# Performance work log

Hardware: AMD Instinct MI355X
Metric: run time of the kernel (lower is better)

## Reference

```python
import jax, jax.numpy as jnp
import numpy as np
from jax import lax

N_NODES = 100000
N_EDGES = 600000  # even: edges stored as consecutive reverse pairs
NODE_F = 64
EDGE_F = 16
EDGE_H = 128
NODE_H = 128
NUM_STEPS = 6


def setup_inputs() -> dict:
    key = jax.random.key(0)
    ks = jax.random.split(key, 16)
    # paired reverse edges: edge 2k is (src,dst), edge 2k+1 is (dst,src)
    src = jax.random.randint(ks[0], (N_EDGES // 2,), 0, N_NODES, dtype=jnp.int32)
    dst = jax.random.randint(ks[1], (N_EDGES // 2,), 0, N_NODES, dtype=jnp.int32)
    from_nodes = jnp.stack([src, dst], axis=1).reshape(-1)
    to_nodes = jnp.stack([dst, src], axis=1).reshape(-1)
    edges = jnp.stack([from_nodes, to_nodes], axis=0)
    return {
        "node_features": jax.random.normal(ks[2], (N_NODES, NODE_F), jnp.float32),
        "edge_features": jax.random.normal(ks[3], (N_EDGES, EDGE_F), jnp.float32),
        "edge_hiddens": jnp.zeros((N_EDGES, EDGE_H), jnp.float32),
        "edges": edges,
        "W1_w": jax.random.normal(ks[4], (NODE_F, EDGE_H), jnp.float32) / np.sqrt(NODE_F),
        "W1_b": jnp.zeros((EDGE_H,), jnp.float32),
        "W2_w": jax.random.normal(ks[5], (EDGE_F, EDGE_H), jnp.float32) / np.sqrt(EDGE_F),
        "W2_b": jnp.zeros((EDGE_H,), jnp.float32),
        "W3_w": jax.random.normal(ks[6], (EDGE_H, EDGE_H), jnp.float32) / np.sqrt(EDGE_H),
        "W3_b": jnp.zeros((EDGE_H,), jnp.float32),
        "U1_w": jax.random.normal(ks[7], (NODE_F, NODE_H), jnp.float32) / np.sqrt(NODE_F),
        "U1_b": jnp.zeros((NODE_H,), jnp.float32),
        "U2_w": jax.random.normal(ks[8], (EDGE_H, NODE_H), jnp.float32) / np.sqrt(EDGE_H),
        "U2_b": jnp.zeros((NODE_H,), jnp.float32),
    }


def reference(node_features, edge_features, edge_hiddens, edges,
              W1_w, W1_b, W2_w, W2_b, W3_w, W3_b, U1_w, U1_b, U2_w, U2_b):
    from_nodes = edges[0]
    to_nodes = edges[1]
    n_edges = edges.shape[1]
    # backlink of edge i is its reverse pair: even i -> i+1, odd i -> i-1
    idx = jnp.arange(n_edges)
    backlink = idx + ((idx + 1) % 2) * 2 - 1

    # loop-invariant terms
    W1_x_u = (node_features @ W1_w + W1_b)[from_nodes]     # [E, EH]
    W2_x_uv = edge_features @ W2_w + W2_b                  # [E, EH]

    def step(h, _):
        # sum edge hiddens by source node, gather back per-edge, drop backlink
        s = jax.ops.segment_sum(h, from_nodes, num_segments=N_NODES)  # [N, EH]
        wu = s[from_nodes] - h[backlink]                               # [E, EH]
        h_new = jax.nn.relu(W1_x_u + W2_x_uv + (wu @ W3_w + W3_b))
        return h_new, None

    edge_h, _ = lax.scan(step, edge_hiddens, None, length=NUM_STEPS)

    U1_x_u = node_features @ U1_w + U1_b                   # [N, NH]
    U2_vu = edge_h @ U2_w + U2_b                           # [E, NH]
    agg = jax.ops.segment_sum(U2_vu, to_nodes, num_segments=N_NODES)
    node_hiddens = jax.nn.relu(U1_x_u + agg)               # [N, NH]
    return node_hiddens
```

## Files before the change

### kernel.cpp

```cpp
#include <hip/hip_runtime.h>
#include <hip/hip_bf16.h>

#define N_NODES 100000
#define N_EDGES 600000
#define SCAN_BLOCKS ((N_NODES + 255) / 256)

typedef __bf16 bf16;
typedef __bf16 bf16x2 __attribute__((ext_vector_type(2)));
typedef __bf16 bf16x4 __attribute__((ext_vector_type(4)));
typedef __bf16 bf16x8 __attribute__((ext_vector_type(8)));
typedef float f32x4 __attribute__((ext_vector_type(4)));

__global__ void deg_hist(const int* __restrict__ from, int* __restrict__ deg, int E) {
    int e = blockIdx.x * blockDim.x + threadIdx.x;
    if (e < E) atomicAdd(&deg[from[e]], 1);
}

__global__ __launch_bounds__(256) void block_sums(
    const int* __restrict__ deg, int* __restrict__ bsum)
{
    __shared__ int s[256];
    int i = blockIdx.x * 256 + threadIdx.x;
    s[threadIdx.x] = (i < N_NODES) ? deg[i] : 0;
    __syncthreads();
    for (int st = 128; st > 0; st >>= 1) {
        if (threadIdx.x < st) s[threadIdx.x] += s[threadIdx.x + st];
        __syncthreads();
    }
    if (threadIdx.x == 0) bsum[blockIdx.x] = s[0];
}

__global__ __launch_bounds__(256) void scan_partials(
    const int* __restrict__ bsum, int* __restrict__ bpref, int* __restrict__ off)
{
    __shared__ int s[SCAN_BLOCKS];
    for (int i = threadIdx.x; i < SCAN_BLOCKS; i += 256) s[i] = bsum[i];
    __syncthreads();
    if (threadIdx.x == 0) {
        int run = 0;
        for (int i = 0; i < SCAN_BLOCKS; i++) { int t = s[i]; s[i] = run; run += t; }
        off[N_NODES] = run;
    }
    __syncthreads();
    for (int i = threadIdx.x; i < SCAN_BLOCKS; i += 256) bpref[i] = s[i];
}

__global__ __launch_bounds__(256) void block_scan(
    const int* __restrict__ deg, const int* __restrict__ bpref,
    int* __restrict__ off, int* __restrict__ cursor)
{
    __shared__ int s[256];
    int i = blockIdx.x * 256 + threadIdx.x;
    int v = (i < N_NODES) ? deg[i] : 0;
    s[threadIdx.x] = v;
    __syncthreads();
    for (int st = 1; st < 256; st <<= 1) {
        int x = (threadIdx.x >= st) ? s[threadIdx.x - st] : 0;
        __syncthreads();
        s[threadIdx.x] += x;
        __syncthreads();
    }
    if (i < N_NODES) {
        int o = bpref[blockIdx.x] + s[threadIdx.x] - v;
        off[i] = o;
        cursor[i] = o;
    }
}

__global__ void scatter_csr(const int* __restrict__ from, int* __restrict__ cursor,
                            int* __restrict__ se, int* __restrict__ rank, int E) {
    int e = blockIdx.x * blockDim.x + threadIdx.x;
    if (e < E) {
        int p = atomicAdd(&cursor[from[e]], 1);
        se[p] = e;
        rank[e] = p;
    }
}

__global__ void make_maps(const int* __restrict__ se, const int* __restrict__ from,
                          const int* __restrict__ rank,
                          int* __restrict__ fromP, int* __restrict__ backP, int E) {
    int i = blockIdx.x * blockDim.x + threadIdx.x;
    if (i < E) {
        int e = se[i];
        fromP[i] = from[e];
        backP[i] = rank[e ^ 1];
    }
}

__global__ __launch_bounds__(256) void node_gemm(
    const float* __restrict__ A, const float* __restrict__ B,
    const float* __restrict__ bias, float* __restrict__ C, int M)
{
    __shared__ float As[16][65];
    __shared__ float Bs[16][128];
    int row0 = blockIdx.x * 64;
    int tid = threadIdx.x;
    int tx = tid & 15, ty = tid >> 4;
    float acc[4][8];
    #pragma unroll
    for (int i = 0; i < 4; i++)
        #pragma unroll
        for (int j = 0; j < 8; j++) acc[i][j] = 0.f;

    for (int kk = 0; kk < 64; kk += 16) {
        int m  = tid >> 2;
        int k4 = (tid & 3) * 4;
        float4 v = make_float4(0.f, 0.f, 0.f, 0.f);
        if (row0 + m < M)
            v = *(const float4*)(A + (size_t)(row0 + m) * 64 + kk + k4);
        As[k4 + 0][m] = v.x; As[k4 + 1][m] = v.y;
        As[k4 + 2][m] = v.z; As[k4 + 3][m] = v.w;
        #pragma unroll
        for (int t = 0; t < 2; t++) {
            int id = tid + t * 256;
            int k = id >> 5, n4 = (id & 31) * 4;
            *(float4*)(&Bs[k][n4]) = *(const float4*)(B + (size_t)(kk + k) * 128 + n4);
        }
        __syncthreads();
        #pragma unroll
        for (int k = 0; k < 16; k++) {
            float a[4], b[8];
            #pragma unroll
            for (int i = 0; i < 4; i++) a[i] = As[k][ty * 4 + i];
            #pragma unroll
            for (int j = 0; j < 8; j++) b[j] = Bs[k][tx + j * 16];
            #pragma unroll
            for (int i = 0; i < 4; i++)
                #pragma unroll
                for (int j = 0; j < 8; j++) acc[i][j] += a[i] * b[j];
        }
        __syncthreads();
    }
    #pragma unroll
    for (int i = 0; i < 4; i++) {
        int r = row0 + ty * 4 + i;
        if (r < M) {
            #pragma unroll
            for (int j = 0; j < 8; j++) {
                int c = tx + j * 16;
                C[(size_t)r * 128 + c] = acc[i][j] + bias[c];
            }
        }
    }
}

__global__ __launch_bounds__(256) void base_sorted(
    const float* __restrict__ nodeW1, const int* __restrict__ fromP,
    const int* __restrict__ se, const float* __restrict__ ef,
    const float* __restrict__ W2, const float* __restrict__ W2b,
    const float* __restrict__ W3b, bf16* __restrict__ baseP)
{
    int tid = threadIdx.x;
    int c0 = (tid & 31) * 4;
    int sub = tid >> 5;
    float4 w[16];
    #pragma unroll
    for (int k = 0; k < 16; k++) w[k] = *(const float4*)(W2 + k * 128 + c0);
    float4 bias;
    {
        float4 a = *(const float4*)(W2b + c0);
        float4 b = *(const float4*)(W3b + c0);
        bias = make_float4(a.x + b.x, a.y + b.y, a.z + b.z, a.w + b.w);
    }
    #pragma unroll 1
    for (int it = 0; it < 64; ++it) {
        int i = blockIdx.x * 512 + it * 8 + sub;
        if (i >= N_EDGES) break;
        const float* efr = ef + (size_t)se[i] * 16;
        float4 nv = *(const float4*)(nodeW1 + (size_t)fromP[i] * 128 + c0);
        float4 acc = make_float4(bias.x + nv.x, bias.y + nv.y,
                                 bias.z + nv.z, bias.w + nv.w);
        #pragma unroll
        for (int k = 0; k < 16; k++) {
            float s = efr[k];
            acc.x += s * w[k].x; acc.y += s * w[k].y;
            acc.z += s * w[k].z; acc.w += s * w[k].w;
        }
        bf16x4 o;
        o[0] = (bf16)acc.x; o[1] = (bf16)acc.y; o[2] = (bf16)acc.z; o[3] = (bf16)acc.w;
        *(bf16x4*)(baseP + (size_t)i * 128 + c0) = o;
    }
}

__global__ __launch_bounds__(256) void prep_weights(
    const float* __restrict__ W3, const float* __restrict__ U2,
    bf16* __restrict__ W3T, bf16* __restrict__ U2T)
{
    int i = blockIdx.x * 256 + threadIdx.x;
    if (i < 128 * 128) {
        int k = i >> 7, n = i & 127;
        W3T[n * 128 + k] = (bf16)W3[k * 128 + n];
        U2T[n * 128 + k] = (bf16)U2[k * 128 + n];
    }
}

__global__ __launch_bounds__(256) void edge_mfma_v2(
    const bf16* __restrict__ baseP, const bf16* __restrict__ gin,
    const bf16* __restrict__ S, const int* __restrict__ fromP,
    const int* __restrict__ backP, const bf16* __restrict__ BT,
    bf16* __restrict__ gout, int fused)
{
    __shared__ bf16 Bsw[128 * 128];
    int tid = threadIdx.x;

    #pragma unroll
    for (int t = 0; t < 8; t++) {
        int c = tid + t * 256;
        int cmr = c & 15;
        int cq  = (c >> 4) & 3;
        int ckt = (c >> 6) & 3;
        int cn  = c >> 8;
        int brow = cn * 16 + cmr;
        int bcol = ckt * 32 + cq * 8;
        *(bf16x8*)&Bsw[(size_t)c * 8] =
            *(const bf16x8*)(BT + (size_t)brow * 128 + bcol);
    }
    __syncthreads();

    int wave = tid >> 6, lane = tid & 63;
    int quad = lane >> 4, mr = lane & 15;

    #pragma unroll 1
    for (int it = 0; it < 4; ++it) {
        int i0 = blockIdx.x * 256 + wave * 64 + it * 16;
        if (i0 >= N_EDGES) break;
        int i = i0 + mr;

        bf16x8 afr[4];
        if (!fused) {
            #pragma unroll
            for (int kt = 0; kt < 4; kt++) {
                bf16x8 bb = *(const bf16x8*)(baseP + (size_t)i * 128 + kt * 32 + quad * 8);
                #pragma unroll
                for (int j = 0; j < 8; j++)
                    afr[kt][j] = (bf16)fmaxf((float)bb[j], 0.f);
            }
        } else {
            const bf16* sr = S   + (size_t)fromP[i] * 128;
            const bf16* gr = gin + (size_t)backP[i] * 128;
            #pragma unroll
            for (int kt = 0; kt < 4; kt++) {
                int c = kt * 32 + quad * 8;
                bf16x8 bb = *(const bf16x8*)(baseP + (size_t)i * 128 + c);
                bf16x8 gg = *(const bf16x8*)(gr + c);
                bf16x8 ss = *(const bf16x8*)(sr + c);
                #pragma unroll
                for (int j = 0; j < 8; j++) {
                    float v = (float)bb[j] + (float)ss[j] - (float)gg[j];
                    afr[kt][j] = (bf16)fmaxf(v, 0.f);
                }
            }
        }

        f32x4 acc[8];
        #pragma unroll
        for (int n = 0; n < 8; n++) acc[n] = (f32x4){0.f, 0.f, 0.f, 0.f};
        #pragma unroll
        for (int kt = 0; kt < 4; kt++) {
            #pragma unroll
            for (int n = 0; n < 8; n++) {
                bf16x8 b = *(const bf16x8*)&Bsw[(size_t)(((n * 4 + kt) * 64) + lane) * 8];
                acc[n] = __builtin_amdgcn_mfma_f32_16x16x32_bf16(afr[kt], b, acc[n], 0, 0, 0);
            }
        }

        #pragma unroll
        for (int np = 0; np < 4; np++) {
            int n0 = np * 2;
            #pragma unroll
            for (int reg = 0; reg < 4; reg++) {
                float v0 = acc[n0][reg], v1 = acc[n0 + 1][reg];
                float o0 = __shfl_xor(v0, 1);
                float o1 = __shfl_xor(v1, 1);
                bf16x2 pk;
                int colb;
                if ((mr & 1) == 0) {
                    pk[0] = (bf16)v0; pk[1] = (bf16)o0;
                    colb = n0 * 16 + mr;
                } else {
                    pk[0] = (bf16)o1; pk[1] = (bf16)v1;
                    colb = (n0 + 1) * 16 + (mr ^ 1);
                }
                int row = i0 + quad * 4 + reg;
                *(bf16x2*)(gout + (size_t)row * 128 + colb) = pk;
            }
        }
    }
}

__global__ __launch_bounds__(256) void segsum_stream(
    const bf16* __restrict__ g, const int* __restrict__ off, bf16* __restrict__ S)
{
    int n = blockIdx.x * 4 + (threadIdx.x >> 6);
    if (n >= N_NODES) return;
    int lane = threadIdx.x & 63;
    int o0 = off[n], o1 = off[n + 1];
    float a0 = 0.f, a1 = 0.f;
    for (int i = o0; i < o1; ++i) {
        bf16x2 v = *(const bf16x2*)(g + (size_t)i * 128 + lane * 2);
        a0 += (float)v[0];
        a1 += (float)v[1];
    }
    bf16x2 o; o[0] = (bf16)a0; o[1] = (bf16)a1;
    *(bf16x2*)(S + (size_t)n * 128 + lane * 2) = o;
}

__global__ __launch_bounds__(256) void segsum_final(
    const bf16* __restrict__ g, const int* __restrict__ off,
    const int* __restrict__ backP, float* __restrict__ agg)
{
    int n = blockIdx.x * 4 + (threadIdx.x >> 6);
    if (n >= N_NODES) return;
    int lane = threadIdx.x & 63;
    int o0 = off[n], o1 = off[n + 1];
    float a0 = 0.f, a1 = 0.f;
    for (int i = o0; i < o1; ++i) {
        int e = backP[i];
        bf16x2 v = *(const bf16x2*)(g + (size_t)e * 128 + lane * 2);
        a0 += (float)v[0];
        a1 += (float)v[1];
    }
    *(float2*)(agg + (size_t)n * 128 + lane * 2) = make_float2(a0, a1);
}

__global__ __launch_bounds__(256) void final_out(
    const float* __restrict__ U1x, const float* __restrict__ agg,
    const int* __restrict__ deg, const float* __restrict__ U2b,
    float* __restrict__ out)
{
    int gid = blockIdx.x * 256 + threadIdx.x;
    int n  = gid >> 5;
    if (n >= N_NODES) return;
    int c4 = gid & 31;
    float d = (float)deg[n];
    float4 a  = *(const float4*)(U1x + (size_t)n * 128 + c4 * 4);
    float4 ag = *(const float4*)(agg + (size_t)n * 128 + c4 * 4);
    float4 ub = *(const float4*)(U2b + c4 * 4);
    float4 r;
    r.x = fmaxf(a.x + ag.x + d * ub.x, 0.f);
    r.y = fmaxf(a.y + ag.y + d * ub.y, 0.f);
    r.z = fmaxf(a.z + ag.z + d * ub.z, 0.f);
    r.w = fmaxf(a.w + ag.w + d * ub.w, 0.f);
    *(float4*)(out + (size_t)n * 128 + c4 * 4) = r;
}

extern "C" void kernel_launch(void* const* d_in, const int* in_sizes, int n_in,
                              void* d_out, int out_size, void* d_ws, size_t ws_size,
                              hipStream_t stream) {
    const float* nf  = (const float*)d_in[0];
    const float* ef  = (const float*)d_in[1];
    const int* edges = (const int*)d_in[3];
    const int* from  = edges;
    const float* W1w = (const float*)d_in[4];
    const float* W1b = (const float*)d_in[5];
    const float* W2w = (const float*)d_in[6];
    const float* W2b = (const float*)d_in[7];
    const float* W3w = (const float*)d_in[8];
    const float* W3b = (const float*)d_in[9];
    const float* U1w = (const float*)d_in[10];
    const float* U1b = (const float*)d_in[11];
    const float* U2w = (const float*)d_in[12];
    const float* U2b = (const float*)d_in[13];
    float* out = (float*)d_out;

    const size_t NODE_MAT = (size_t)N_NODES * 128;
    const size_t EDGE_MAT = (size_t)N_EDGES * 128;
    char* w = (char*)d_ws;
    float* nodeW1 = (float*)w; w += NODE_MAT * 4;
    float* agg    = (float*)w; w += NODE_MAT * 4;
    bf16*  S      = (bf16*)w;  w += NODE_MAT * 2;
    bf16*  baseP  = (bf16*)w;  w += EDGE_MAT * 2;
    bf16*  g0     = (bf16*)w;  w += EDGE_MAT * 2;
    bf16*  g1     = (bf16*)w;  w += EDGE_MAT * 2;
    bf16*  W3T    = (bf16*)w;  w += 128 * 128 * 2;
    bf16*  U2T    = (bf16*)w;  w += 128 * 128 * 2;
    int*   deg    = (int*)w;   w += (size_t)N_NODES * 4;
    int*   off    = (int*)w;   w += (size_t)(N_NODES + 1) * 4;
    int*   cursor = (int*)w;   w += (size_t)N_NODES * 4;
    int*   bsum   = (int*)w;   w += (size_t)SCAN_BLOCKS * 4;
    int*   bpref  = (int*)w;   w += (size_t)SCAN_BLOCKS * 4;
    int*   se     = (int*)w;   w += (size_t)N_EDGES * 4;
    int*   rank   = (int*)w;   w += (size_t)N_EDGES * 4;
    int*   fromP  = (int*)w;   w += (size_t)N_EDGES * 4;
    int*   backP  = (int*)w;   w += (size_t)N_EDGES * 4;

    hipMemsetAsync(deg, 0, (size_t)N_NODES * 4, stream);
    deg_hist<<<(N_EDGES + 255) / 256, 256, 0, stream>>>(from, deg, N_EDGES);
    block_sums<<<SCAN_BLOCKS, 256, 0, stream>>>(deg, bsum);
    scan_partials<<<1, 256, 0, stream>>>(bsum, bpref, off);
    block_scan<<<SCAN_BLOCKS, 256, 0, stream>>>(deg, bpref, off, cursor);
    scatter_csr<<<(N_EDGES + 255) / 256, 256, 0, stream>>>(from, cursor, se, rank, N_EDGES);
    make_maps<<<(N_EDGES + 255) / 256, 256, 0, stream>>>(se, from, rank, fromP, backP, N_EDGES);

    prep_weights<<<(128 * 128 + 255) / 256, 256, 0, stream>>>(W3w, U2w, W3T, U2T);
    node_gemm<<<(N_NODES + 63) / 64, 256, 0, stream>>>(nf, W1w, W1b, nodeW1, N_NODES);
    base_sorted<<<(N_EDGES + 511) / 512, 256, 0, stream>>>(
        nodeW1, fromP, se, ef, W2w, W2b, W3b, baseP);

    const int EGRID = (N_EDGES + 255) / 256;
    bf16* G[2] = {g0, g1};
    edge_mfma_v2<<<EGRID, 256, 0, stream>>>(
        baseP, G[0], S, fromP, backP, W3T, G[0], 0);
    segsum_stream<<<(N_NODES + 3) / 4, 256, 0, stream>>>(G[0], off, S);
    int cur = 0;
    for (int it = 1; it < 5; ++it) {
        edge_mfma_v2<<<EGRID, 256, 0, stream>>>(
            baseP, G[cur], S, fromP, backP, W3T, G[cur ^ 1], 1);
        cur ^= 1;
        segsum_stream<<<(N_NODES + 3) / 4, 256, 0, stream>>>(G[cur], off, S);
    }
    edge_mfma_v2<<<EGRID, 256, 0, stream>>>(
        baseP, G[cur], S, fromP, backP, U2T, G[cur ^ 1], 1);
    cur ^= 1;
    segsum_final<<<(N_NODES + 3) / 4, 256, 0, stream>>>(G[cur], off, backP, agg);

    node_gemm<<<(N_NODES + 63) / 64, 256, 0, stream>>>(nf, U1w, U1b, nodeW1, N_NODES);
    final_out<<<(N_NODES * 32 + 255) / 256, 256, 0, stream>>>(nodeW1, agg, deg, U2b, out);
}
```

Before: 1.657 ms.

## Widen edge MFMA blocks, prefetch indices, vectorize segsum, fuse final aggregation

```diff
diff --git a/kernel.cpp b/kernel.cpp
--- a/kernel.cpp
+++ b/kernel.cpp
@@ -195,7 +195,7 @@
     }
 }
 
-__global__ __launch_bounds__(256) void edge_mfma_v2(
+__global__ __launch_bounds__(512) void edge_mfma_v9(
     const bf16* __restrict__ baseP, const bf16* __restrict__ gin,
     const bf16* __restrict__ S, const int* __restrict__ fromP,
     const int* __restrict__ backP, const bf16* __restrict__ BT,
@@ -205,8 +205,8 @@
     int tid = threadIdx.x;
 
     #pragma unroll
-    for (int t = 0; t < 8; t++) {
-        int c = tid + t * 256;
+    for (int t = 0; t < 4; t++) {
+        int c = tid + t * 512;
         int cmr = c & 15;
         int cq  = (c >> 4) & 3;
         int ckt = (c >> 6) & 3;
@@ -220,12 +220,19 @@
 
     int wave = tid >> 6, lane = tid & 63;
     int quad = lane >> 4, mr = lane & 15;
+    int ibase = blockIdx.x * 512 + wave * 64;
+    if (ibase >= N_EDGES) return;
+
+    int frc = 0, bkc = 0;
+    if (fused) { frc = fromP[ibase + mr]; bkc = backP[ibase + mr]; }
 
     #pragma unroll 1
     for (int it = 0; it < 4; ++it) {
-        int i0 = blockIdx.x * 256 + wave * 64 + it * 16;
-        if (i0 >= N_EDGES) break;
+        int i0 = ibase + it * 16;
         int i = i0 + mr;
+
+        int frn = 0, bkn = 0;
+        if (fused && it < 3) { frn = fromP[i + 16]; bkn = backP[i + 16]; }
 
         bf16x8 afr[4];
         if (!fused) {
@@ -237,8 +244,8 @@
                     afr[kt][j] = (bf16)fmaxf((float)bb[j], 0.f);
             }
         } else {
-            const bf16* sr = S   + (size_t)fromP[i] * 128;
-            const bf16* gr = gin + (size_t)backP[i] * 128;
+            const bf16* sr = S   + (size_t)frc * 128;
+            const bf16* gr = gin + (size_t)bkc * 128;
             #pragma unroll
             for (int kt = 0; kt < 4; kt++) {
                 int c = kt * 32 + quad * 8;
@@ -286,63 +293,66 @@
                 *(bf16x2*)(gout + (size_t)row * 128 + colb) = pk;
             }
         }
-    }
-}
-
-__global__ __launch_bounds__(256) void segsum_stream(
+
+        frc = frn; bkc = bkn;
+    }
+}
+
+__global__ __launch_bounds__(256) void segsum_stream2(
     const bf16* __restrict__ g, const int* __restrict__ off, bf16* __restrict__ S)
 {
     int n = blockIdx.x * 4 + (threadIdx.x >> 6);
     if (n >= N_NODES) return;
     int lane = threadIdx.x & 63;
+    int half = lane >> 5;
+    int c4 = (lane & 31) * 4;
     int o0 = off[n], o1 = off[n + 1];
-    float a0 = 0.f, a1 = 0.f;
-    for (int i = o0; i < o1; ++i) {
-        bf16x2 v = *(const bf16x2*)(g + (size_t)i * 128 + lane * 2);
-        a0 += (float)v[0];
-        a1 += (float)v[1];
-    }
-    bf16x2 o; o[0] = (bf16)a0; o[1] = (bf16)a1;
-    *(bf16x2*)(S + (size_t)n * 128 + lane * 2) = o;
-}
-
-__global__ __launch_bounds__(256) void segsum_final(
-    const bf16* __restrict__ g, const int* __restrict__ off,
-    const int* __restrict__ backP, float* __restrict__ agg)
+    float a0 = 0.f, a1 = 0.f, a2 = 0.f, a3 = 0.f;
+    for (int p = o0 + half; p < o1; p += 2) {
+        bf16x4 v = *(const bf16x4*)(g + (size_t)p * 128 + c4);
+        a0 += (float)v[0]; a1 += (float)v[1];
+        a2 += (float)v[2]; a3 += (float)v[3];
+    }
+    a0 += __shfl_xor(a0, 32); a1 += __shfl_xor(a1, 32);
+    a2 += __shfl_xor(a2, 32); a3 += __shfl_xor(a3, 32);
+    if (half == 0) {
+        bf16x4 o;
+        o[0] = (bf16)a0; o[1] = (bf16)a1; o[2] = (bf16)a2; o[3] = (bf16)a3;
+        *(bf16x4*)(S + (size_t)n * 128 + c4) = o;
+    }
+}
+
+__global__ __launch_bounds__(256) void final_gather_out(
+    const bf16* __restrict__ gB, const int* __restrict__ off,
+    const int* __restrict__ backP, const float* __restrict__ U1x,
+    const float* __restrict__ U2b, float* __restrict__ out)
 {
     int n = blockIdx.x * 4 + (threadIdx.x >> 6);
     if (n >= N_NODES) return;
     int lane = threadIdx.x & 63;
+    int half = lane >> 5;
+    int c4 = (lane & 31) * 4;
     int o0 = off[n], o1 = off[n + 1];
-    float a0 = 0.f, a1 = 0.f;
-    for (int i = o0; i < o1; ++i) {
-        int e = backP[i];
-        bf16x2 v = *(const bf16x2*)(g + (size_t)e * 128 + lane * 2);
-        a0 += (float)v[0];
-        a1 += (float)v[1];
-    }
-    *(float2*)(agg + (size_t)n * 128 + lane * 2) = make_float2(a0, a1);
-}
-
-__global__ __launch_bounds__(256) void final_out(
-    const float* __restrict__ U1x, const float* __restrict__ agg,
-    const int* __restrict__ deg, const float* __restrict__ U2b,
-    float* __restrict__ out)
-{
-    int gid = blockIdx.x * 256 + threadIdx.x;
-    int n  = gid >> 5;
-    if (n >= N_NODES) return;
-    int c4 = gid & 31;
-    float d = (float)deg[n];
-    float4 a  = *(const float4*)(U1x + (size_t)n * 128 + c4 * 4);
-    float4 ag = *(const float4*)(agg + (size_t)n * 128 + c4 * 4);
-    float4 ub = *(const float4*)(U2b + c4 * 4);
-    float4 r;
-    r.x = fmaxf(a.x + ag.x + d * ub.x, 0.f);
-    r.y = fmaxf(a.y + ag.y + d * ub.y, 0.f);
-    r.z = fmaxf(a.z + ag.z + d * ub.z, 0.f);
-    r.w = fmaxf(a.w + ag.w + d * ub.w, 0.f);
-    *(float4*)(out + (size_t)n * 128 + c4 * 4) = r;
+    float a0 = 0.f, a1 = 0.f, a2 = 0.f, a3 = 0.f;
+    for (int p = o0 + half; p < o1; p += 2) {
+        int e = backP[p];
+        bf16x4 v = *(const bf16x4*)(gB + (size_t)e * 128 + c4);
+        a0 += (float)v[0]; a1 += (float)v[1];
+        a2 += (float)v[2]; a3 += (float)v[3];
+    }
+    a0 += __shfl_xor(a0, 32); a1 += __shfl_xor(a1, 32);
+    a2 += __shfl_xor(a2, 32); a3 += __shfl_xor(a3, 32);
+    if (half == 0) {
+        float d = (float)(o1 - o0);
+        float4 u = *(const float4*)(U1x + (size_t)n * 128 + c4);
+        float4 b = *(const float4*)(U2b + c4);
+        float4 r;
+        r.x = fmaxf(u.x + a0 + d * b.x, 0.f);
+        r.y = fmaxf(u.y + a1 + d * b.y, 0.f);
+        r.z = fmaxf(u.z + a2 + d * b.z, 0.f);
+        r.w = fmaxf(u.w + a3 + d * b.w, 0.f);
+        *(float4*)(out + (size_t)n * 128 + c4) = r;
+    }
 }
 
 extern "C" void kernel_launch(void* const* d_in, const int* in_sizes, int n_in,
@@ -368,7 +378,6 @@
     const size_t EDGE_MAT = (size_t)N_EDGES * 128;
     char* w = (char*)d_ws;
     float* nodeW1 = (float*)w; w += NODE_MAT * 4;
-    float* agg    = (float*)w; w += NODE_MAT * 4;
     bf16*  S      = (bf16*)w;  w += NODE_MAT * 2;
     bf16*  baseP  = (bf16*)w;  w += EDGE_MAT * 2;
     bf16*  g0     = (bf16*)w;  w += EDGE_MAT * 2;
@@ -398,23 +407,25 @@
     base_sorted<<<(N_EDGES + 511) / 512, 256, 0, stream>>>(
         nodeW1, fromP, se, ef, W2w, W2b, W3b, baseP);
 
-    const int EGRID = (N_EDGES + 255) / 256;
+    const int EGRID = (N_EDGES + 511) / 512;
+    const int SGRID = (N_NODES + 3) / 4;
     bf16* G[2] = {g0, g1};
-    edge_mfma_v2<<<EGRID, 256, 0, stream>>>(
+
+    edge_mfma_v9<<<EGRID, 512, 0, stream>>>(
         baseP, G[0], S, fromP, backP, W3T, G[0], 0);
-    segsum_stream<<<(N_NODES + 3) / 4, 256, 0, stream>>>(G[0], off, S);
+    segsum_stream2<<<SGRID, 256, 0, stream>>>(G[0], off, S);
     int cur = 0;
     for (int it = 1; it < 5; ++it) {
-        edge_mfma_v2<<<EGRID, 256, 0, stream>>>(
+        edge_mfma_v9<<<EGRID, 512, 0, stream>>>(
             baseP, G[cur], S, fromP, backP, W3T, G[cur ^ 1], 1);
         cur ^= 1;
-        segsum_stream<<<(N_NODES + 3) / 4, 256, 0, stream>>>(G[cur], off, S);
-    }
-    edge_mfma_v2<<<EGRID, 256, 0, stream>>>(
+        segsum_stream2<<<SGRID, 256, 0, stream>>>(G[cur], off, S);
+    }
+    edge_mfma_v9<<<EGRID, 512, 0, stream>>>(
         baseP, G[cur], S, fromP, backP, U2T, G[cur ^ 1], 1);
     cur ^= 1;
-    segsum_final<<<(N_NODES + 3) / 4, 256, 0, stream>>>(G[cur], off, backP, agg);
 
     node_gemm<<<(N_NODES + 63) / 64, 256, 0, stream>>>(nf, U1w, U1b, nodeW1, N_NODES);
-    final_out<<<(N_NODES * 32 + 255) / 256, 256, 0, stream>>>(nodeW1, agg, deg, U2b, out);
-}
+    final_gather_out<<<SGRID, 256, 0, stream>>>(
+        G[cur], off, backP, nodeW1, U2b, out);
+}
```

Result: faster. 1.559 ms (-5.9%).
